# Kernel optimization log

Measured on AMD Instinct MI355X. Metric: run time of the kernel, lower is better.

## Reference

```python
import jax, jax.numpy as jnp
import numpy as np

N = 102400      # total nodes
E = 1638400     # total edges (avg degree 16)
B = 2048        # number of graphs
DIN = 128       # input feature dim
K = 30          # sort-pool k


def setup_inputs() -> dict:
    key = jax.random.key(0)
    ks = jax.random.split(key, 16)
    x = jax.random.normal(ks[0], (N, DIN), dtype=jnp.float32)
    edge_index = jax.random.randint(ks[1], (2, E), 0, N)
    batch = jnp.sort(jax.random.randint(ks[2], (N,), 0, B))

    def w(k, sh):
        return jax.random.normal(k, sh, dtype=jnp.float32) * 0.1

    return {
        "x": x, "edge_index": edge_index, "batch": batch,
        "W1": w(ks[3], (DIN, 32)), "b1": w(ks[4], (32,)),
        "W2": w(ks[5], (32, 32)), "b2": w(ks[6], (32,)),
        "W3": w(ks[7], (32, 32)), "b3": w(ks[8], (32,)),
        "W4": w(ks[9], (32, 1)), "b4": w(ks[10], (1,)),
        "conv1_w": w(ks[11], (16, 1, 97)), "conv1_b": w(ks[11], (16,)),
        "conv2_w": w(ks[12], (32, 16, 5)), "conv2_b": w(ks[12], (32,)),
        "lin1_w": w(ks[13], (352, 128)), "lin1_b": w(ks[13], (128,)),
        "lin2_w": w(ks[14], (128, 1)), "lin2_b": w(ks[14], (1,)),
    }


def _gcn(x, W, b, src, dst, dinv, n):
    # PyG GCNConv: D^{-1/2}(A+I)D^{-1/2} X W + b, transform first (small out dim)
    h = x @ W
    msg = h[src] * (dinv[src] * dinv[dst])[:, None]            # [E, F]
    agg = jax.ops.segment_sum(msg, dst, num_segments=n)        # neighbor aggregation
    agg = agg + h * (dinv * dinv)[:, None]                     # self-loop term (norm = 1/deg)
    return agg + b


def _sort_pool(h, batch, num_graphs, k):
    # global_sort_pool: per-graph descending sort by last channel, keep top-k, zero-pad
    n, f = h.shape
    order = jnp.lexsort((-h[:, -1], batch))                    # primary: graph id, secondary: -key
    hs, bs = h[order], batch[order]
    counts = jax.ops.segment_sum(jnp.ones(n, jnp.int32), batch, num_segments=num_graphs)
    starts = jnp.cumsum(counts) - counts                       # exclusive prefix
    pos = jnp.arange(n) - starts[bs]                           # rank within graph
    keep = pos < k
    out = jnp.zeros((num_graphs, k, f), h.dtype)
    out = out.at[bs, jnp.clip(pos, 0, k - 1)].add(jnp.where(keep[:, None], hs, 0.0))
    return out.reshape(num_graphs, k * f)


def _conv1d(x, w, b, stride):
    y = jax.lax.conv_general_dilated(x, w, (stride,), 'VALID',
                                     dimension_numbers=('NCH', 'OIH', 'NCH'))
    return y + b[None, :, None]


def reference(x, edge_index, batch, W1, b1, W2, b2, W3, b3, W4, b4,
              conv1_w, conv1_b, conv2_w, conv2_b, lin1_w, lin1_b, lin2_w, lin2_b):
    n = x.shape[0]
    src, dst = edge_index[0], edge_index[1]
    deg = jax.ops.segment_sum(jnp.ones(src.shape[0], x.dtype), dst, num_segments=n) + 1.0
    dinv = jax.lax.rsqrt(deg)

    h1 = jnp.tanh(_gcn(x, W1, b1, src, dst, dinv, n))
    h2 = jnp.tanh(_gcn(h1, W2, b2, src, dst, dinv, n))
    h3 = jnp.tanh(_gcn(h2, W3, b3, src, dst, dinv, n))
    h4 = jnp.tanh(_gcn(h3, W4, b4, src, dst, dinv, n))
    h = jnp.concatenate([h1, h2, h3, h4], axis=-1)             # [N, 97]

    h = _sort_pool(h, batch, B, K)                             # [B, 2910]
    h = h[:, None, :]                                          # [B, 1, 2910]
    h = jax.nn.relu(_conv1d(h, conv1_w, conv1_b, 97))          # [B, 16, 30]
    bsz, c, l = h.shape
    h = h.reshape(bsz, c, l // 2, 2).max(axis=-1)              # maxpool(2,2) -> [B,16,15]
    h = jax.nn.relu(_conv1d(h, conv2_w, conv2_b, 1))           # [B, 32, 11]
    h = h.reshape(bsz, -1)                                     # [B, 352]
    h = jax.nn.relu(h @ lin1_w + lin1_b)
    # Dropout(0.5) is identity at inference
    return jax.nn.sigmoid(h @ lin2_w + lin2_b)                 # [B, 1]
```

## Files before the change

### kernel.cpp

```cpp
#include <hip/hip_runtime.h>
#include <math.h>

#define NN 102400
#define NE 1638400
#define NG 2048
#define KTOP 30
#define NBUCK 400
#define EPB 4096
#define NB1 400
#define GPB 2

__global__ __launch_bounds__(256) void fused_front_kernel(
    const int* __restrict__ dst, int* __restrict__ hist1,
    const float* __restrict__ x, const float* __restrict__ W1,
    float* __restrict__ htmp,
    const int* __restrict__ batch, int* __restrict__ starts) {
    __shared__ float Wsh[128 * 32];
    __shared__ int hsh[NBUCK];
    int bid = blockIdx.x;
    int tid = threadIdx.x;

    if (bid < NB1) {
        for (int q = tid; q < NBUCK; q += 256) hsh[q] = 0;
        __syncthreads();
        const int4* dp = (const int4*)(dst + bid * EPB);
        for (int i4 = tid; i4 < EPB / 4; i4 += 256) {
            int4 dd = dp[i4];
            atomicAdd(&hsh[dd.x >> 8], 1);
            atomicAdd(&hsh[dd.y >> 8], 1);
            atomicAdd(&hsh[dd.z >> 8], 1);
            atomicAdd(&hsh[dd.w >> 8], 1);
        }
        __syncthreads();
        for (int q = tid; q < NBUCK; q += 256) hist1[q * NB1 + bid] = hsh[q];
    } else if (bid < NB1 + 800) {
        int bidx = bid - NB1;
        for (int i = tid; i < 128 * 32; i += 256) Wsh[i] = W1[i];
        __syncthreads();
        int jb = (tid >> 6) << 3;
        int q = tid & 63;
        int n0 = bidx * 128 + q;
        int n1 = n0 + 64;
        const float* x0p = x + (size_t)n0 * 128;
        const float* x1p = x + (size_t)n1 * 128;
        float acc0[8], acc1[8];
#pragma unroll
        for (int j = 0; j < 8; ++j) { acc0[j] = 0.f; acc1[j] = 0.f; }
#pragma unroll 2
        for (int k = 0; k < 128; k += 4) {
            float4 xa = *(const float4*)(x0p + k);
            float4 xb = *(const float4*)(x1p + k);
            float xs0[4] = {xa.x, xa.y, xa.z, xa.w};
            float xs1[4] = {xb.x, xb.y, xb.z, xb.w};
#pragma unroll
            for (int kk = 0; kk < 4; ++kk) {
                float4 wlo = *(const float4*)&Wsh[(k + kk) * 32 + jb];
                float4 whi = *(const float4*)&Wsh[(k + kk) * 32 + jb + 4];
                float v0 = xs0[kk], v1 = xs1[kk];
                acc0[0] += v0 * wlo.x; acc0[1] += v0 * wlo.y;
                acc0[2] += v0 * wlo.z; acc0[3] += v0 * wlo.w;
                acc0[4] += v0 * whi.x; acc0[5] += v0 * whi.y;
                acc0[6] += v0 * whi.z; acc0[7] += v0 * whi.w;
                acc1[0] += v1 * wlo.x; acc1[1] += v1 * wlo.y;
                acc1[2] += v1 * wlo.z; acc1[3] += v1 * wlo.w;
                acc1[4] += v1 * whi.x; acc1[5] += v1 * whi.y;
                acc1[6] += v1 * whi.z; acc1[7] += v1 * whi.w;
            }
        }
        float4 o0 = {acc0[0], acc0[1], acc0[2], acc0[3]};
        float4 o1 = {acc0[4], acc0[5], acc0[6], acc0[7]};
        float4 o2 = {acc1[0], acc1[1], acc1[2], acc1[3]};
        float4 o3 = {acc1[4], acc1[5], acc1[6], acc1[7]};
        *(float4*)&htmp[(size_t)n0 * 32 + jb] = o0;
        *(float4*)&htmp[(size_t)n0 * 32 + jb + 4] = o1;
        *(float4*)&htmp[(size_t)n1 * 32 + jb] = o2;
        *(float4*)&htmp[(size_t)n1 * 32 + jb + 4] = o3;
    } else {
        int i = (bid - NB1 - 800) * 256 + tid;
        if (i < NN) {
            int c = batch[i];
            int p = (i == 0) ? -1 : batch[i - 1];
            for (int g = p + 1; g <= c; ++g) starts[g] = i;
            if (i == NN - 1) {
                for (int g = c + 1; g <= NG; ++g) starts[g] = NN;
            }
        }
    }
}

__global__ __launch_bounds__(256) void s1a_kernel(const int* __restrict__ hist1,
                                                  int* __restrict__ offs,
                                                  int* __restrict__ totals) {
    __shared__ int A[512], B[512];
    int q = blockIdx.x, tid = threadIdx.x;
    int i0 = tid, i1 = tid + 256;
    int v0 = (i0 < NB1) ? hist1[q * NB1 + i0] : 0;
    int v1 = (i1 < NB1) ? hist1[q * NB1 + i1] : 0;
    A[i0] = v0; A[i1] = v1;
    __syncthreads();
    int* cur = A; int* nxt = B;
    for (int off = 1; off < 512; off <<= 1) {
        nxt[i0] = cur[i0] + ((i0 >= off) ? cur[i0 - off] : 0);
        nxt[i1] = cur[i1] + cur[i1 - off];
        __syncthreads();
        int* t = cur; cur = nxt; nxt = t;
    }
    if (i0 < NB1) offs[q * NB1 + i0] = cur[i0] - v0;
    if (i1 < NB1) offs[q * NB1 + i1] = cur[i1] - v1;
    if (tid == 0) totals[q] = cur[511];
}

__global__ __launch_bounds__(256) void s1b_kernel(const int* __restrict__ totals,
                                                  int* __restrict__ bucketStart,
                                                  int* __restrict__ rowptr) {
    __shared__ int A[512], B[512];
    int tid = threadIdx.x;
    int i0 = tid, i1 = tid + 256;
    int v0 = (i0 < NBUCK) ? totals[i0] : 0;
    int v1 = (i1 < NBUCK) ? totals[i1] : 0;
    A[i0] = v0; A[i1] = v1;
    __syncthreads();
    int* cur = A; int* nxt = B;
    for (int off = 1; off < 512; off <<= 1) {
        nxt[i0] = cur[i0] + ((i0 >= off) ? cur[i0 - off] : 0);
        nxt[i1] = cur[i1] + cur[i1 - off];
        __syncthreads();
        int* t = cur; cur = nxt; nxt = t;
    }
    if (i0 < NBUCK) bucketStart[i0] = cur[i0] - v0;
    if (i1 < NBUCK) bucketStart[i1] = cur[i1] - v1;
    if (tid == 0) { bucketStart[NBUCK] = cur[511]; rowptr[NN] = cur[511]; }
}

__global__ __launch_bounds__(256) void p1_kernel(const int* __restrict__ src,
                                                 const int* __restrict__ dst,
                                                 const int* __restrict__ offs,
                                                 const int* __restrict__ bucketStart,
                                                 unsigned int* __restrict__ ebuf) {
    __shared__ int myoff[NBUCK];
    int b = blockIdx.x, tid = threadIdx.x;
    for (int q = tid; q < NBUCK; q += 256)
        myoff[q] = bucketStart[q] + offs[q * NB1 + b];
    __syncthreads();
    const int4* dp = (const int4*)(dst + b * EPB);
    const int4* sp = (const int4*)(src + b * EPB);
    for (int i4 = tid; i4 < EPB / 4; i4 += 256) {
        int4 dd = dp[i4];
        int4 ss = sp[i4];
        int p0 = atomicAdd(&myoff[dd.x >> 8], 1);
        int p1 = atomicAdd(&myoff[dd.y >> 8], 1);
        int p2 = atomicAdd(&myoff[dd.z >> 8], 1);
        int p3 = atomicAdd(&myoff[dd.w >> 8], 1);
        ebuf[p0] = ((unsigned int)(dd.x & 255) << 24) | (unsigned int)ss.x;
        ebuf[p1] = ((unsigned int)(dd.y & 255) << 24) | (unsigned int)ss.y;
        ebuf[p2] = ((unsigned int)(dd.z & 255) << 24) | (unsigned int)ss.z;
        ebuf[p3] = ((unsigned int)(dd.w & 255) << 24) | (unsigned int)ss.w;
    }
}

__global__ __launch_bounds__(256) void p2_kernel(const unsigned int* __restrict__ ebuf,
                                                 const int* __restrict__ bucketStart,
                                                 int* __restrict__ csr_src,
                                                 int* __restrict__ rowptr,
                                                 float* __restrict__ dinv) {
    __shared__ int fcnt[256];
    __shared__ int tmp[256];
    __shared__ int foff[256];
    int q = blockIdx.x, tid = threadIdx.x;
    int base = bucketStart[q];
    int ecnt = bucketStart[q + 1] - base;
    fcnt[tid] = 0;
    __syncthreads();
    for (int i = tid; i < ecnt; i += 256) {
        unsigned int e = ebuf[base + i];
        atomicAdd(&fcnt[e >> 24], 1);
    }
    __syncthreads();
    int c = fcnt[tid];
    int n = q * 256 + tid;
    dinv[n] = rsqrtf((float)c + 1.0f);
    tmp[tid] = c;
    __syncthreads();
    for (int off = 1; off < 256; off <<= 1) {
        int u = (tid >= off) ? tmp[tid - off] : 0;
        __syncthreads();
        tmp[tid] += u;
        __syncthreads();
    }
    int excl = base + tmp[tid] - c;
    rowptr[n] = excl;
    foff[tid] = excl;
    __syncthreads();
    for (int i = tid; i < ecnt; i += 256) {
        unsigned int e = ebuf[base + i];
        int pos = atomicAdd(&foff[e >> 24], 1);
        csr_src[pos] = (int)(e & 0xFFFFFF);
    }
}


template <int NEXT>
__global__ __launch_bounds__(256) void gcn_aggd_kernel(
    const int* __restrict__ rowptr, const int* __restrict__ csr_src,
    const float* __restrict__ htmp, const float* __restrict__ dinv,
    const float* __restrict__ b, const float* __restrict__ Wn,
    float* __restrict__ hout, float* __restrict__ htn) {
    __shared__ float Ws[32 * 32];
    __shared__ float Hs[32][36];
    int tid = threadIdx.x;
    if (NEXT == 32) {
        for (int i = tid; i < 1024; i += 256) Ws[i] = Wn[i];
    } else {
        if (tid < 32) Ws[tid] = Wn[tid];
    }
    int idx = blockIdx.x * 256 + tid;
    int n = idx >> 3, fg = (idx & 7) << 2;
    int beg = rowptr[n], end = rowptr[n + 1];
    float di = dinv[n];
    float4 acc = {0.f, 0.f, 0.f, 0.f};
    int i = beg;
    for (; i + 7 < end; i += 8) {
        int s[8];
#pragma unroll
        for (int k = 0; k < 8; ++k) s[k] = csr_src[i + k];
        float c[8];
#pragma unroll
        for (int k = 0; k < 8; ++k) c[k] = dinv[s[k]] * di;
        float4 v[8];
#pragma unroll
        for (int k = 0; k < 8; ++k) v[k] = *(const float4*)&htmp[(size_t)s[k] * 32 + fg];
#pragma unroll
        for (int k = 0; k < 8; ++k) {
            acc.x += v[k].x * c[k]; acc.y += v[k].y * c[k];
            acc.z += v[k].z * c[k]; acc.w += v[k].w * c[k];
        }
    }
    for (; i + 3 < end; i += 4) {
        int s0 = csr_src[i], s1 = csr_src[i + 1];
        int s2 = csr_src[i + 2], s3 = csr_src[i + 3];
        float c0 = dinv[s0] * di, c1 = dinv[s1] * di;
        float c2 = dinv[s2] * di, c3 = dinv[s3] * di;
        float4 v0 = *(const float4*)&htmp[(size_t)s0 * 32 + fg];
        float4 v1 = *(const float4*)&htmp[(size_t)s1 * 32 + fg];
        float4 v2 = *(const float4*)&htmp[(size_t)s2 * 32 + fg];
        float4 v3 = *(const float4*)&htmp[(size_t)s3 * 32 + fg];
        acc.x += v0.x * c0; acc.y += v0.y * c0; acc.z += v0.z * c0; acc.w += v0.w * c0;
        acc.x += v1.x * c1; acc.y += v1.y * c1; acc.z += v1.z * c1; acc.w += v1.w * c1;
        acc.x += v2.x * c2; acc.y += v2.y * c2; acc.z += v2.z * c2; acc.w += v2.w * c2;
        acc.x += v3.x * c3; acc.y += v3.y * c3; acc.z += v3.z * c3; acc.w += v3.w * c3;
    }
    for (; i < end; ++i) {
        int s = csr_src[i];
        float c = dinv[s] * di;
        float4 v = *(const float4*)&htmp[(size_t)s * 32 + fg];
        acc.x += v.x * c; acc.y += v.y * c; acc.z += v.z * c; acc.w += v.w * c;
    }
    float dd = di * di;
    float4 hs = *(const float4*)&htmp[(size_t)n * 32 + fg];
    float4 bb = *(const float4*)&b[fg];
    float4 o;
    o.x = tanhf(acc.x + hs.x * dd + bb.x);
    o.y = tanhf(acc.y + hs.y * dd + bb.y);
    o.z = tanhf(acc.z + hs.z * dd + bb.z);
    o.w = tanhf(acc.w + hs.w * dd + bb.w);
    *(float4*)&hout[(size_t)n * 32 + fg] = o;
    int nl = tid >> 3;
    *(float4*)&Hs[nl][fg] = o;
    __syncthreads();
    if (NEXT == 32) {
        int n2 = tid >> 3, j4 = (tid & 7) << 2;
        int gnode = blockIdx.x * 32 + n2;
        float4 r = {0.f, 0.f, 0.f, 0.f};
#pragma unroll
        for (int k = 0; k < 32; ++k) {
            float h = Hs[n2][k];
            float4 wv = *(const float4*)&Ws[k * 32 + j4];
            r.x += h * wv.x; r.y += h * wv.y; r.z += h * wv.z; r.w += h * wv.w;
        }
        *(float4*)&htn[(size_t)gnode * 32 + j4] = r;
    } else {
        if (tid < 32) {
            int gnode = blockIdx.x * 32 + tid;
            float s = 0.f;
#pragma unroll
            for (int k = 0; k < 32; ++k) s += Hs[tid][k] * Ws[k];
            htn[gnode] = s;
        }
    }
}

__global__ __launch_bounds__(256) void gcn_agg1_kernel(
    const int* __restrict__ rowptr, const int* __restrict__ csr_src,
    const float* __restrict__ htmp, const float* __restrict__ dinv,
    const float* __restrict__ b, float* __restrict__ hout) {
    int n = blockIdx.x * blockDim.x + threadIdx.x;
    if (n >= NN) return;
    int beg = rowptr[n], end = rowptr[n + 1];
    float di = dinv[n];
    float acc = 0.f;
    int i = beg;
    for (; i + 7 < end; i += 8) {
        int s[8];
#pragma unroll
        for (int k = 0; k < 8; ++k) s[k] = csr_src[i + k];
        float c[8], v[8];
#pragma unroll
        for (int k = 0; k < 8; ++k) c[k] = dinv[s[k]] * di;
#pragma unroll
        for (int k = 0; k < 8; ++k) v[k] = htmp[s[k]];
#pragma unroll
        for (int k = 0; k < 8; ++k) acc += v[k] * c[k];
    }
    for (; i < end; ++i) {
        int s = csr_src[i];
        acc += htmp[s] * (dinv[s] * di);
    }
    hout[n] = tanhf(acc + htmp[n] * di * di + b[0]);
}


__global__ __launch_bounds__(256) void pool_cnn_kernel(
    const float* __restrict__ h1, const float* __restrict__ h2,
    const float* __restrict__ h3, const float* __restrict__ h4,
    const int* __restrict__ starts,
    const float* __restrict__ c1w, const float* __restrict__ c1b,
    const float* __restrict__ c2w, const float* __restrict__ c2b,
    const float* __restrict__ l1w, const float* __restrict__ l1b,
    const float* __restrict__ l2w, const float* __restrict__ l2b,
    float* __restrict__ out) {
    __shared__ float Psh[GPB * 3000];
    __shared__ float CW[16 * 100];
    __shared__ float KY[GPB * 480];
    int tid = threadIdx.x;
    int gg = tid >> 7;
    int lt = tid & 127;
    int g = blockIdx.x * GPB + gg;
    float* P  = Psh + gg * 3000;
    float* ky = KY + gg * 480;
    float* y2 = P;
    float* y3 = P + 240;
    float* z  = P + 592;

    int start = starts[g];
    int end = starts[g + 1];
    int cnt = end - start;

    for (int i = lt; i < 3000; i += 128) P[i] = 0.f;
    for (int i = tid; i < 16 * 97; i += 256) {
        int c = i / 97, f = i % 97;
        CW[c * 100 + f] = c1w[i];
    }
    bool fits = (cnt <= 480);
    if (fits) {
        for (int i = lt; i < cnt; i += 128) ky[i] = h4[start + i];
    }
    __syncthreads();

    for (int i = lt; i < cnt; i += 128) {
        float key = fits ? ky[i] : h4[start + i];
        int rank = 0;
        if (fits) {
            for (int j = 0; j < cnt; ++j) {
                float kj = ky[j];
                rank += (kj > key) || (kj == key && j < i);
            }
        } else {
            for (int j = 0; j < cnt; ++j) {
                float kj = h4[start + j];
                rank += (kj > key) || (kj == key && j < i);
            }
        }
        if (rank < KTOP) {
            int node = start + i;
            const float4* r1 = (const float4*)(h1 + (size_t)node * 32);
            const float4* r2 = (const float4*)(h2 + (size_t)node * 32);
            const float4* r3 = (const float4*)(h3 + (size_t)node * 32);
            float* Pr = P + rank * 100;
#pragma unroll
            for (int q = 0; q < 8; ++q) *(float4*)&Pr[4 * q] = r1[q];
#pragma unroll
            for (int q = 0; q < 8; ++q) *(float4*)&Pr[32 + 4 * q] = r2[q];
#pragma unroll
            for (int q = 0; q < 8; ++q) *(float4*)&Pr[64 + 4 * q] = r3[q];
            Pr[96] = key;
        }
    }
    __syncthreads();

    for (int o = lt; o < 16 * KTOP; o += 128) {
        int t = o >> 4, c = o & 15;
        float s = c1b[c];
        const float* Pr = P + t * 100;
        const float* Wr = &CW[c * 100];
#pragma unroll
        for (int f4 = 0; f4 < 24; ++f4) {
            float4 pv = *(const float4*)(Pr + 4 * f4);
            float4 wv = *(const float4*)(Wr + 4 * f4);
            s += wv.x * pv.x; s += wv.y * pv.y; s += wv.z * pv.z; s += wv.w * pv.w;
        }
        s += Wr[96] * Pr[96];
        ky[c * KTOP + t] = fmaxf(s, 0.f);
    }
    __syncthreads();

    for (int o = lt; o < 16 * 15; o += 128) {
        int c = o / 15, t = o % 15;
        y2[o] = fmaxf(ky[c * KTOP + 2 * t], ky[c * KTOP + 2 * t + 1]);
    }
    __syncthreads();

    for (int o = lt; o < 32 * 11; o += 128) {
        int c = o / 11, t = o % 11;
        float s = c2b[c];
#pragma unroll
        for (int i = 0; i < 16; ++i)
#pragma unroll
            for (int j = 0; j < 5; ++j)
                s += c2w[(c * 16 + i) * 5 + j] * y2[i * 15 + t + j];
        y3[o] = fmaxf(s, 0.f);
    }
    __syncthreads();

    {
        int o = lt;
        float s = l1b[o];
#pragma unroll 16
        for (int i = 0; i < 352; ++i) s += y3[i] * l1w[i * 128 + o];
        z[o] = fmaxf(s, 0.f);
    }
    __syncthreads();

    if (lt == 0) {
        float s = l2b[0];
#pragma unroll 4
        for (int i = 0; i < 128; ++i) s += z[i] * l2w[i];
        out[g] = 1.f / (1.f + expf(-s));
    }
}

extern "C" void kernel_launch(void* const* d_in, const int* in_sizes, int n_in,
                              void* d_out, int out_size, void* d_ws, size_t ws_size,
                              hipStream_t stream) {
    const float* x   = (const float*)d_in[0];
    const int* ei    = (const int*)d_in[1];
    const int* batch = (const int*)d_in[2];
    const float* W1  = (const float*)d_in[3];
    const float* b1  = (const float*)d_in[4];
    const float* W2  = (const float*)d_in[5];
    const float* b2  = (const float*)d_in[6];
    const float* W3  = (const float*)d_in[7];
    const float* b3  = (const float*)d_in[8];
    const float* W4  = (const float*)d_in[9];
    const float* b4  = (const float*)d_in[10];
    const float* c1w = (const float*)d_in[11];
    const float* c1b = (const float*)d_in[12];
    const float* c2w = (const float*)d_in[13];
    const float* c2b = (const float*)d_in[14];
    const float* l1w = (const float*)d_in[15];
    const float* l1b = (const float*)d_in[16];
    const float* l2w = (const float*)d_in[17];
    const float* l2b = (const float*)d_in[18];
    float* out = (float*)d_out;

    const int* srcp = ei;
    const int* dstp = ei + NE;

    char* w = (char*)d_ws;
    float* dinv      = (float*)w;               w += sizeof(float) * NN;
    float* htmpA     = (float*)w;               w += sizeof(float) * NN * 32;
    float* htmpB     = (float*)w;               w += sizeof(float) * NN * 32;
    float* h1        = (float*)w;               w += sizeof(float) * NN * 32;
    float* h2        = (float*)w;               w += sizeof(float) * NN * 32;
    float* h3        = (float*)w;               w += sizeof(float) * NN * 32;
    float* h4        = (float*)w;               w += sizeof(float) * NN;
    int*   rowptr    = (int*)w;                 w += sizeof(int) * (NN + 1);
    int*   hist1     = (int*)w;                 w += sizeof(int) * NBUCK * NB1;
    int*   offs      = (int*)w;                 w += sizeof(int) * NBUCK * NB1;
    int*   totals    = (int*)w;                 w += sizeof(int) * NBUCK;
    int*   bucketStart = (int*)w;               w += sizeof(int) * (NBUCK + 1);
    int*   csr_src   = (int*)w;                 w += sizeof(int) * NE;
    int*   starts    = (int*)w;                 w += sizeof(int) * (NG + 1);

    unsigned int* ebuf = (unsigned int*)h2;

    fused_front_kernel<<<NB1 + 800 + 400, 256, 0, stream>>>(dstp, hist1, x, W1, htmpA,
                                                            batch, starts);
    s1a_kernel<<<NBUCK, 256, 0, stream>>>(hist1, offs, totals);
    s1b_kernel<<<1, 256, 0, stream>>>(totals, bucketStart, rowptr);
    p1_kernel<<<NB1, 256, 0, stream>>>(srcp, dstp, offs, bucketStart, ebuf);
    p2_kernel<<<NBUCK, 256, 0, stream>>>(ebuf, bucketStart, csr_src, rowptr, dinv);

    gcn_aggd_kernel<32><<<NN / 32, 256, 0, stream>>>(rowptr, csr_src, htmpA, dinv, b1,
                                                     W2, h1, htmpB);
    gcn_aggd_kernel<32><<<NN / 32, 256, 0, stream>>>(rowptr, csr_src, htmpB, dinv, b2,
                                                     W3, h2, htmpA);
    gcn_aggd_kernel<1><<<NN / 32, 256, 0, stream>>>(rowptr, csr_src, htmpA, dinv, b3,
                                                    W4, h3, htmpB);
    gcn_agg1_kernel<<<NN / 256, 256, 0, stream>>>(rowptr, csr_src, htmpB, dinv, b4, h4);

    pool_cnn_kernel<<<NG / GPB, 256, 0, stream>>>(h1, h2, h3, h4, starts,
                                                  c1w, c1b, c2w, c2b,
                                                  l1w, l1b, l2w, l2b, out);
}
```

Measured before the change: 247.1 us.

## Pool one graph per block and gather selected rows cooperatively

The pool+CNN kernel now handles one graph per 256-thread block instead of two graphs per block with 128 threads each, launching NG blocks. Top-k selection first records the chosen node indices and keys in shared memory. All threads then gather the 24 float4 chunks of each selected row in parallel, instead of one thread copying a whole row. This spreads the rank and gather work over more threads and grid blocks, but the tail stages (linear layers) leave more threads idle per block.

```diff
diff --git a/kernel.cpp b/kernel.cpp
--- a/kernel.cpp
+++ b/kernel.cpp
@@ -8,7 +8,6 @@
 #define NBUCK 400
 #define EPB 4096
 #define NB1 400
-#define GPB 2
 
 __global__ __launch_bounds__(256) void fused_front_kernel(
     const int* __restrict__ dst, int* __restrict__ hist1,
@@ -198,7 +197,6 @@
     }
 }
 
-
 template <int NEXT>
 __global__ __launch_bounds__(256) void gcn_aggd_kernel(
     const int* __restrict__ rowptr, const int* __restrict__ csr_src,
@@ -319,6 +317,8 @@
 }
 
 
+#define PSTR 100
+
 __global__ __launch_bounds__(256) void pool_cnn_kernel(
     const float* __restrict__ h1, const float* __restrict__ h2,
     const float* __restrict__ h3, const float* __restrict__ h4,
@@ -328,40 +328,39 @@
     const float* __restrict__ l1w, const float* __restrict__ l1b,
     const float* __restrict__ l2w, const float* __restrict__ l2b,
     float* __restrict__ out) {
-    __shared__ float Psh[GPB * 3000];
-    __shared__ float CW[16 * 100];
-    __shared__ float KY[GPB * 480];
+    __shared__ float P[KTOP][PSTR];
+    __shared__ float CW[16 * PSTR];
+    __shared__ float KY[480];
+    __shared__ int   sel_node[KTOP];
+    __shared__ float sel_key[KTOP];
+    float* keys = KY;
+    float* y2 = &P[0][0];
+    float* y3 = &P[0][0] + 240;
+    float* z  = &P[0][0] + 592;
+    int g = blockIdx.x;
     int tid = threadIdx.x;
-    int gg = tid >> 7;
-    int lt = tid & 127;
-    int g = blockIdx.x * GPB + gg;
-    float* P  = Psh + gg * 3000;
-    float* ky = KY + gg * 480;
-    float* y2 = P;
-    float* y3 = P + 240;
-    float* z  = P + 592;
 
     int start = starts[g];
     int end = starts[g + 1];
     int cnt = end - start;
 
-    for (int i = lt; i < 3000; i += 128) P[i] = 0.f;
+    for (int i = tid; i < KTOP * PSTR; i += 256) (&P[0][0])[i] = 0.f;
     for (int i = tid; i < 16 * 97; i += 256) {
         int c = i / 97, f = i % 97;
-        CW[c * 100 + f] = c1w[i];
+        CW[c * PSTR + f] = c1w[i];
     }
     bool fits = (cnt <= 480);
     if (fits) {
-        for (int i = lt; i < cnt; i += 128) ky[i] = h4[start + i];
-    }
-    __syncthreads();
-
-    for (int i = lt; i < cnt; i += 128) {
-        float key = fits ? ky[i] : h4[start + i];
+        for (int i = tid; i < cnt; i += 256) keys[i] = h4[start + i];
+    }
+    __syncthreads();
+
+    for (int i = tid; i < cnt; i += 256) {
+        float key = fits ? keys[i] : h4[start + i];
         int rank = 0;
         if (fits) {
             for (int j = 0; j < cnt; ++j) {
-                float kj = ky[j];
+                float kj = keys[j];
                 rank += (kj > key) || (kj == key && j < i);
             }
         } else {
@@ -371,27 +370,29 @@
             }
         }
         if (rank < KTOP) {
-            int node = start + i;
-            const float4* r1 = (const float4*)(h1 + (size_t)node * 32);
-            const float4* r2 = (const float4*)(h2 + (size_t)node * 32);
-            const float4* r3 = (const float4*)(h3 + (size_t)node * 32);
-            float* Pr = P + rank * 100;
-#pragma unroll
-            for (int q = 0; q < 8; ++q) *(float4*)&Pr[4 * q] = r1[q];
-#pragma unroll
-            for (int q = 0; q < 8; ++q) *(float4*)&Pr[32 + 4 * q] = r2[q];
-#pragma unroll
-            for (int q = 0; q < 8; ++q) *(float4*)&Pr[64 + 4 * q] = r3[q];
-            Pr[96] = key;
-        }
-    }
-    __syncthreads();
-
-    for (int o = lt; o < 16 * KTOP; o += 128) {
+            sel_node[rank] = start + i;
+            sel_key[rank] = key;
+        }
+    }
+    __syncthreads();
+
+    int nsel = (cnt < KTOP) ? cnt : KTOP;
+    for (int u = tid; u < nsel * 24; u += 256) {
+        int r = u / 24, q = u % 24;
+        int node = sel_node[r];
+        const float* srcp = (q < 8) ? h1 : (q < 16) ? h2 : h3;
+        int qq = q & 7;
+        float4 v = *(const float4*)(srcp + (size_t)node * 32 + 4 * qq);
+        *(float4*)&P[r][(q < 8 ? 0 : (q < 16 ? 32 : 64)) + 4 * qq] = v;
+    }
+    for (int r = tid; r < nsel; r += 256) P[r][96] = sel_key[r];
+    __syncthreads();
+
+    for (int o = tid; o < 16 * KTOP; o += 256) {
         int t = o >> 4, c = o & 15;
         float s = c1b[c];
-        const float* Pr = P + t * 100;
-        const float* Wr = &CW[c * 100];
+        const float* Pr = &P[t][0];
+        const float* Wr = &CW[c * PSTR];
 #pragma unroll
         for (int f4 = 0; f4 < 24; ++f4) {
             float4 pv = *(const float4*)(Pr + 4 * f4);
@@ -399,17 +400,17 @@
             s += wv.x * pv.x; s += wv.y * pv.y; s += wv.z * pv.z; s += wv.w * pv.w;
         }
         s += Wr[96] * Pr[96];
-        ky[c * KTOP + t] = fmaxf(s, 0.f);
-    }
-    __syncthreads();
-
-    for (int o = lt; o < 16 * 15; o += 128) {
+        KY[c * KTOP + t] = fmaxf(s, 0.f);
+    }
+    __syncthreads();
+
+    for (int o = tid; o < 16 * 15; o += 256) {
         int c = o / 15, t = o % 15;
-        y2[o] = fmaxf(ky[c * KTOP + 2 * t], ky[c * KTOP + 2 * t + 1]);
-    }
-    __syncthreads();
-
-    for (int o = lt; o < 32 * 11; o += 128) {
+        y2[o] = fmaxf(KY[c * KTOP + 2 * t], KY[c * KTOP + 2 * t + 1]);
+    }
+    __syncthreads();
+
+    for (int o = tid; o < 32 * 11; o += 256) {
         int c = o / 11, t = o % 11;
         float s = c2b[c];
 #pragma unroll
@@ -421,8 +422,7 @@
     }
     __syncthreads();
 
-    {
-        int o = lt;
+    for (int o = tid; o < 128; o += 256) {
         float s = l1b[o];
 #pragma unroll 16
         for (int i = 0; i < 352; ++i) s += y3[i] * l1w[i * 128 + o];
@@ -430,7 +430,7 @@
     }
     __syncthreads();
 
-    if (lt == 0) {
+    if (tid == 0) {
         float s = l2b[0];
 #pragma unroll 4
         for (int i = 0; i < 128; ++i) s += z[i] * l2w[i];
@@ -498,7 +498,7 @@
                                                     W4, h3, htmpB);
     gcn_agg1_kernel<<<NN / 256, 256, 0, stream>>>(rowptr, csr_src, htmpB, dinv, b4, h4);
 
-    pool_cnn_kernel<<<NG / GPB, 256, 0, stream>>>(h1, h2, h3, h4, starts,
-                                                  c1w, c1b, c2w, c2b,
-                                                  l1w, l1b, l2w, l2b, out);
-}
+    pool_cnn_kernel<<<NG, 256, 0, stream>>>(h1, h2, h3, h4, starts,
+                                            c1w, c1b, c2w, c2b,
+                                            l1w, l1b, l2w, l2b, out);
+}
```

New measurement: 244.0 us. No clear change (-1.2%).
